# Kernel optimization log

Measured on AMD Instinct MI355X. Metric: run time of the kernel, lower is better.

Reference implementation:

```python
import math
import jax, jax.numpy as jnp
import numpy as np

B, LA, LB, H = 16, 1024, 1024, 512
NEG = -10000000.0


def setup_inputs() -> dict:
    key = jax.random.key(0)
    k1, k2, k3, k4 = jax.random.split(key, 4)
    a = jax.random.normal(k1, (B, LA, H), dtype=jnp.float32)
    b = jax.random.normal(k2, (B, LB, H), dtype=jnp.float32)
    mask_a = jax.random.randint(k3, (B, LA, 1), 0, 2, dtype=jnp.int32)
    mask_b = jax.random.randint(k4, (B, LB, 1), 0, 2, dtype=jnp.int32)
    temperature = jnp.asarray(1.0 / math.sqrt(H), dtype=jnp.float32)
    return {"a": a, "b": b, "mask_a": mask_a, "mask_b": mask_b, "temperature": temperature}


def reference(a, b, mask_a, mask_b, temperature):
    # attn[b,i,j] = <a_i, b_j> * temperature  -> [B, LA, LB]
    attn = jnp.einsum("bid,bjd->bij", a, b) * temperature
    # pairwise validity mask: outer product of per-token masks
    mask = jnp.einsum("bik,bjk->bij", mask_a.astype(jnp.float32), mask_b.astype(jnp.float32)) > 0
    attn = jnp.where(mask, attn, NEG)
    attn_a = jax.nn.softmax(attn, axis=1)  # softmax over a-tokens
    attn_b = jax.nn.softmax(attn, axis=2)  # softmax over b-tokens
    feature_b = jnp.einsum("bij,bid->bjd", attn_a, a)  # [B, LB, H]
    feature_a = jnp.einsum("bij,bjd->bid", attn_b, b)  # [B, LA, H]
    return (feature_a, feature_b)
```

## Files before the change

kernel.cpp:

```cpp
#include <hip/hip_runtime.h>
#include <hip/hip_bf16.h>

#define NB_ 16
#define LA_ 1024
#define LB_ 1024
#define H_  512

typedef __attribute__((ext_vector_type(8))) short short8;
typedef __attribute__((ext_vector_type(4))) float f32x4;

using bf16 = __hip_bfloat16;

__device__ __forceinline__ float bf2f(unsigned short u) {
    union { unsigned int i; float f; } c; c.i = ((unsigned)u) << 16; return c.f;
}
__device__ __forceinline__ unsigned short f2bf(float f) {
    bf16 h = __float2bfloat16(f);
    return *(unsigned short*)&h;
}

__device__ __forceinline__ void load_lds16(const void* g, void* l) {
    __builtin_amdgcn_global_load_lds(
        (const __attribute__((address_space(1))) void*)g,
        (__attribute__((address_space(3))) void*)l, 16, 0, 0);
}

template<int DB, int MODE>
__device__ __forceinline__ void gemm_tile_cnt(
    const unsigned short* __restrict__ gA, const unsigned short* __restrict__ gB,
    int lda, int ldb, size_t ko,
    unsigned short* lds, char* lA, char* lB,
    const int* aoff, const int* boff, f32x4 acc[4][8])
{
    const char* bA = (const char*)lds + DB * 32768;
    const char* bB = (const char*)lds + 65536 + DB * 32768;
    const int nxt = (DB ^ 1) * 32768;
    short8 av[4][2];
#pragma unroll
    for (int p = 0; p < 4; ++p) {
        if (p == 0) {
#pragma unroll
            for (int f = 0; f < 4; f++)
#pragma unroll
                for (int kk = 0; kk < 2; kk++)
                    av[f][kk] = *(const short8*)(bA + (aoff[f] ^ (kk << 6)));
        }
        short8 bv[2][2];
#pragma unroll
        for (int f = 0; f < 2; f++)
#pragma unroll
            for (int kk = 0; kk < 2; kk++)
                bv[f][kk] = *(const short8*)(bB + (boff[p * 2 + f] ^ (kk << 6)));
        if (MODE == 0) {
            if (p == 0) {
                load_lds16(gA + ko,                       lA + nxt);
                load_lds16(gA + ko + (size_t)64 * lda,    lA + nxt + 8192);
            } else if (p == 1) {
                load_lds16(gA + ko + (size_t)128 * lda,   lA + nxt + 16384);
                load_lds16(gA + ko + (size_t)192 * lda,   lA + nxt + 24576);
            } else if (p == 2) {
                load_lds16(gB + ko,                       lB + nxt);
                load_lds16(gB + ko + (size_t)128 * ldb,   lB + nxt + 16384);
            } else {
                load_lds16(gB + ko + (size_t)64 * ldb,    lB + nxt + 8192);
                load_lds16(gB + ko + (size_t)192 * ldb,   lB + nxt + 24576);
            }
        }
        __builtin_amdgcn_s_barrier();
        __builtin_amdgcn_s_setprio(1);
#pragma unroll
        for (int kk = 0; kk < 2; kk++)
#pragma unroll
            for (int f = 0; f < 2; f++)
#pragma unroll
                for (int m = 0; m < 4; m++)
                    acc[m][p * 2 + f] =
                        __builtin_amdgcn_mfma_f32_16x16x32_bf16(
                            av[m][kk], bv[f][kk], acc[m][p * 2 + f], 0, 0, 0);
        __builtin_amdgcn_s_setprio(0);
        if (p == 1) {
            if (MODE == 0) asm volatile("s_waitcnt vmcnt(4)" ::: "memory");
            else           asm volatile("s_waitcnt vmcnt(0)" ::: "memory");
        }
        if (p == 3 && MODE == 0) asm volatile("s_waitcnt vmcnt(2)" ::: "memory");
        if (p < 3 || MODE == 0) __builtin_amdgcn_s_barrier();
    }
}

template<int DB, int MODE>
__device__ __forceinline__ void gemm_tile_drn(
    const unsigned short* __restrict__ gA, const unsigned short* __restrict__ gB,
    int lda, int ldb, size_t ko,
    unsigned short* lds, char* lA, char* lB,
    const int* aoff, const int* boff, f32x4 acc[4][8])
{
    const char* bA = (const char*)lds + DB * 32768;
    const char* bB = (const char*)lds + 65536 + DB * 32768;
    const int nxt = (DB ^ 1) * 32768;
    if (MODE == 0) {
#pragma unroll
        for (int s = 0; s < 4; s++) {
            load_lds16(gA + ko + (size_t)(s * 64) * lda, lA + nxt + s * 8192);
            load_lds16(gB + ko + (size_t)(s * 64) * ldb, lB + nxt + s * 8192);
        }
    }
    short8 av[4][2];
#pragma unroll
    for (int p = 0; p < 4; ++p) {
        if (p == 0) {
#pragma unroll
            for (int f = 0; f < 4; f++)
#pragma unroll
                for (int kk = 0; kk < 2; kk++)
                    av[f][kk] = *(const short8*)(bA + (aoff[f] ^ (kk << 6)));
        }
        short8 bv[2][2];
#pragma unroll
        for (int f = 0; f < 2; f++)
#pragma unroll
            for (int kk = 0; kk < 2; kk++)
                bv[f][kk] = *(const short8*)(bB + (boff[p * 2 + f] ^ (kk << 6)));
        __builtin_amdgcn_s_barrier();
        __builtin_amdgcn_s_setprio(1);
#pragma unroll
        for (int kk = 0; kk < 2; kk++)
#pragma unroll
            for (int f = 0; f < 2; f++)
#pragma unroll
                for (int m = 0; m < 4; m++)
                    acc[m][p * 2 + f] =
                        __builtin_amdgcn_mfma_f32_16x16x32_bf16(
                            av[m][kk], bv[f][kk], acc[m][p * 2 + f], 0, 0, 0);
        __builtin_amdgcn_s_setprio(0);
        if (p < 3) __builtin_amdgcn_s_barrier();
    }
    __syncthreads();
}

template<int SCHED>
__device__ __forceinline__ void gemm_core256(
    const unsigned short* __restrict__ A, const unsigned short* __restrict__ B,
    int lda, int ldb, int K,
    unsigned short* lds, f32x4 acc[4][8])
{
    const int t = threadIdx.x;
    const int w = t >> 6, lane = t & 63;
    const int wr = w >> 1, wc = w & 1;
    const int lm = lane & 15, q = lane >> 4;

    int aoff[4], boff[8];
#pragma unroll
    for (int f = 0; f < 4; f++) {
        const int ra = wr * 64 + f * 16 + lm;
        aoff[f] = ra * 128 + ((q ^ (ra & 7)) << 4);
    }
#pragma unroll
    for (int f = 0; f < 8; f++) {
        const int rb = wc * 128 + f * 16 + lm;
        boff[f] = rb * 128 + ((q ^ (rb & 7)) << 4);
    }

    const int rstep = w * 8 + (lane >> 3);
    const int sc = (lane & 7) ^ (lane >> 3);
    const unsigned short* gA = A + (size_t)rstep * lda + sc * 8;
    const unsigned short* gB = B + (size_t)rstep * ldb + sc * 8;
    char* lA = (char*)lds + w * 1024;
    char* lB = (char*)lds + 65536 + w * 1024;
    const int NT = K >> 6;

    if (SCHED == 0) {
        load_lds16(gA,                       lA);
        load_lds16(gA + (size_t)64 * lda,    lA + 8192);
        load_lds16(gA + (size_t)128 * lda,   lA + 16384);
        load_lds16(gA + (size_t)192 * lda,   lA + 24576);
        load_lds16(gB,                       lB);
        load_lds16(gB + (size_t)128 * ldb,   lB + 16384);
        load_lds16(gB + (size_t)64 * ldb,    lB + 8192);
        load_lds16(gB + (size_t)192 * ldb,   lB + 24576);
        asm volatile("s_waitcnt vmcnt(2)" ::: "memory");
        __builtin_amdgcn_s_barrier();
        int kt = 0;
        for (; kt + 2 < NT; kt += 2) {
            gemm_tile_cnt<0, 0>(gA, gB, lda, ldb, (size_t)(kt + 1) * 64,
                                lds, lA, lB, aoff, boff, acc);
            gemm_tile_cnt<1, 0>(gA, gB, lda, ldb, (size_t)(kt + 2) * 64,
                                lds, lA, lB, aoff, boff, acc);
        }
        gemm_tile_cnt<0, 0>(gA, gB, lda, ldb, (size_t)(NT - 1) * 64,
                            lds, lA, lB, aoff, boff, acc);
        gemm_tile_cnt<1, 1>(gA, gB, lda, ldb, 0, lds, lA, lB, aoff, boff, acc);
    } else {
#pragma unroll
        for (int s = 0; s < 4; s++) {
            load_lds16(gA + (size_t)(s * 64) * lda, lA + s * 8192);
            load_lds16(gB + (size_t)(s * 64) * ldb, lB + s * 8192);
        }
        __syncthreads();
        int kt = 0;
        for (; kt + 2 < NT; kt += 2) {
            gemm_tile_drn<0, 0>(gA, gB, lda, ldb, (size_t)(kt + 1) * 64,
                                lds, lA, lB, aoff, boff, acc);
            gemm_tile_drn<1, 0>(gA, gB, lda, ldb, (size_t)(kt + 2) * 64,
                                lds, lA, lB, aoff, boff, acc);
        }
        gemm_tile_drn<0, 0>(gA, gB, lda, ldb, (size_t)(NT - 1) * 64,
                            lds, lA, lB, aoff, boff, acc);
        gemm_tile_drn<1, 1>(gA, gB, lda, ldb, 0, lds, lA, lB, aoff, boff, acc);
    }
    __syncthreads();
}

__global__ __launch_bounds__(512, 2) void k_gemm_attn(
    const unsigned short* __restrict__ a_bf, const unsigned short* __restrict__ b_bf,
    const int* __restrict__ mask_a, const int* __restrict__ mask_b,
    const float* __restrict__ temp_p,
    unsigned short* __restrict__ E, unsigned short* __restrict__ ET,
    float* __restrict__ l_row, float* __restrict__ l_col)
{
    __shared__ unsigned short lds[65536];

    const int g = blockIdx.x;
    const int batch = g & 15;
    const int qq = g >> 4;
    const int i0 = (qq >> 2) * 256, j0 = (qq & 3) * 256;

    const unsigned short* A = a_bf + (size_t)batch * LA_ * H_ + (size_t)i0 * H_;
    const unsigned short* B = b_bf + (size_t)batch * LB_ * H_ + (size_t)j0 * H_;
    f32x4 acc[4][8];
#pragma unroll
    for (int x = 0; x < 4; x++)
#pragma unroll
        for (int y = 0; y < 8; y++) acc[x][y] = 0;

    gemm_core256<1>(A, B, H_, H_, H_, lds, acc);

    const float temp = temp_p[0];
    const int t = threadIdx.x, w = t >> 6, lane = t & 63;
    const int wr = w >> 1, wc = w & 1, lm = lane & 15, q = lane >> 4;
    const int* map = mask_a + batch * LA_;
    const int* mbp = mask_b + batch * LB_;
    unsigned short* Ep  = E  + (size_t)batch * LA_ * LB_;
    unsigned short* ETp = ET + (size_t)batch * LB_ * LA_;
    float* lrp = l_row + batch * LA_;
    float* lcp = l_col + batch * LB_;

    int mb8[8];
#pragma unroll
    for (int fn = 0; fn < 8; fn++) mb8[fn] = mbp[j0 + wc * 128 + fn * 16 + lm];

#pragma unroll
    for (int fm = 0; fm < 4; fm++) {
        const int ilb = wr * 64 + fm * 16 + q * 4;
        int ma[4];
#pragma unroll
        for (int r = 0; r < 4; r++) ma[r] = map[i0 + ilb + r];
#pragma unroll
        for (int fn = 0; fn < 8; fn++) {
            const int jl = wc * 128 + fn * 16 + lm;
            ushort4 pk;
            unsigned short* pp = (unsigned short*)&pk;
#pragma unroll
            for (int r = 0; r < 4; r++) {
                const float e = (ma[r] && mb8[fn]) ? __expf(acc[fm][fn][r] * temp) : 0.0f;
                acc[fm][fn][r] = e;
                pp[r] = f2bf(e);
                const int il = ilb + r;
                lds[il * 256 + ((((jl >> 3) ^ ((il >> 1) & 15)) << 3) | (jl & 7))] = pp[r];
            }
            *(ushort4*)(ETp + (size_t)(j0 + jl) * LA_ + i0 + ilb) = pk;
        }
    }

#pragma unroll
    for (int fm = 0; fm < 4; fm++)
#pragma unroll
        for (int r = 0; r < 4; r++) {
            float s = 0.0f;
#pragma unroll
            for (int fn = 0; fn < 8; fn++) s += acc[fm][fn][r];
            s += __shfl_xor(s, 1, 16); s += __shfl_xor(s, 2, 16);
            s += __shfl_xor(s, 4, 16); s += __shfl_xor(s, 8, 16);
            if (lm == 0) atomicAdd(&lrp[i0 + wr * 64 + fm * 16 + q * 4 + r], s);
        }
#pragma unroll
    for (int fn = 0; fn < 8; fn++) {
        float s = 0.0f;
#pragma unroll
        for (int fm = 0; fm < 4; fm++)
#pragma unroll
            for (int r = 0; r < 4; r++) s += acc[fm][fn][r];
        s += __shfl_xor(s, 16, 64); s += __shfl_xor(s, 32, 64);
        if (lane < 16) atomicAdd(&lcp[j0 + wc * 128 + fn * 16 + lm], s);
    }

    __syncthreads();
#pragma unroll
    for (int rep = 0; rep < 16; rep++) {
        const int il = (t >> 5) + rep * 16;
        const int c = t & 31;
        const int phys = c ^ ((il >> 1) & 15);
        short8 v = *(const short8*)(lds + il * 256 + phys * 8);
        *(short8*)(Ep + (size_t)(i0 + il) * LB_ + j0 + c * 8) = v;
    }
}

__global__ __launch_bounds__(512, 2) void k_gemm_feat(
    const unsigned short* __restrict__ E, const unsigned short* __restrict__ ET,
    const unsigned short* __restrict__ aT, const unsigned short* __restrict__ bT,
    const int* __restrict__ mask_a, const int* __restrict__ mask_b,
    const int* __restrict__ nA, const int* __restrict__ nB,
    const float* __restrict__ l_row, const float* __restrict__ l_col,
    const float* __restrict__ mean_a, const float* __restrict__ mean_b,
    float* __restrict__ out)
{
    __shared__ unsigned short lds[65536];

    const int g = blockIdx.x;
    const int zc = g & 31;
    const int qq = g >> 5;
    const int n0 = (qq & 1) * 256, m0 = (qq >> 1) * 256;

    const int batch = zc & 15;
    const bool isA = zc < 16;
    const unsigned short* Amat = (isA ? E : ET) + (size_t)batch * 1024 * 1024;
    const unsigned short* Bm   = (isA ? bT : aT) + (size_t)batch * H_ * 1024;
    const int* mp   = (isA ? mask_a : mask_b) + batch * 1024;
    const int nn    = (isA ? nB : nA)[batch];
    const float* sp = (isA ? l_row : l_col) + batch * 1024;
    const float* mv = (isA ? mean_b : mean_a) + batch * H_;
    float* op = out + (isA ? (size_t)0 : (size_t)NB_ * LA_ * H_) + (size_t)batch * 1024 * H_;

    f32x4 acc[4][8];
#pragma unroll
    for (int x = 0; x < 4; x++)
#pragma unroll
        for (int y = 0; y < 8; y++) acc[x][y] = 0;

    gemm_core256<0>(Amat + (size_t)m0 * 1024, Bm + (size_t)n0 * 1024,
                    1024, 1024, 1024, lds, acc);

    const int t = threadIdx.x, w = t >> 6, lane = t & 63;
    const int wr = w >> 1, wc = w & 1, lm = lane & 15, q = lane >> 4;

    float mval[8];
#pragma unroll
    for (int fn = 0; fn < 8; fn++) mval[fn] = mv[n0 + wc * 128 + fn * 16 + lm];

#pragma unroll
    for (int fm = 0; fm < 4; fm++) {
        const int ib = m0 + wr * 64 + fm * 16 + q * 4;
#pragma unroll
        for (int r = 0; r < 4; r++) {
            const int i = ib + r;
            const bool valid = (mp[i] != 0) && (nn > 0);
            const float inv = valid ? 1.0f / sp[i] : 0.0f;
#pragma unroll
            for (int fn = 0; fn < 8; fn++) {
                const int d = n0 + wc * 128 + fn * 16 + lm;
                op[(size_t)i * H_ + d] = valid ? acc[fm][fn][r] * inv : mval[fn];
            }
        }
    }
}

__global__ __launch_bounds__(256) void k_prep(
    const float* __restrict__ a, const float* __restrict__ b,
    unsigned short* __restrict__ aN, unsigned short* __restrict__ bN,
    unsigned short* __restrict__ aT, unsigned short* __restrict__ bT,
    float* __restrict__ mean_a, float* __restrict__ mean_b,
    const int* __restrict__ mask_a, const int* __restrict__ mask_b,
    int* __restrict__ nA, int* __restrict__ nB,
    float* __restrict__ zero_base)
{
    const int g = blockIdx.x, t = threadIdx.x;
    if (g >= 256) {
        const int s = g - 256;
        *(float4*)(zero_base + ((size_t)s * 256 + t) * 4) = make_float4(0, 0, 0, 0);
        const int batch = s & 15, which = s >> 4;
        const int* m = (which ? mask_b : mask_a) + batch * 1024;
        int cnt = m[t] + m[t + 256] + m[t + 512] + m[t + 768];
        __shared__ int red[256];
        red[t] = cnt;
        __syncthreads();
        for (int off = 128; off; off >>= 1) {
            if (t < off) red[t] += red[t + off];
            __syncthreads();
        }
        if (t == 0) (which ? nB : nA)[batch] = red[0];
        return;
    }
    const int dstrip = g & 7, batch = (g >> 3) & 15, sel = g >> 7;
    const float* src = (sel ? b : a) + (size_t)batch * 1024 * H_;
    unsigned short* np = (sel ? bN : aN) + (size_t)batch * 1024 * H_;
    unsigned short* tp = (sel ? bT : aT) + (size_t)batch * H_ * 1024;
    float* mdst = (sel ? mean_b : mean_a) + batch * H_;
    const int d0 = dstrip * 64;

    __shared__ unsigned short lds[64][68];
    __shared__ float cs[4][64];
    const int c4 = (t & 15) * 4;
    float colsum[4] = {0.f, 0.f, 0.f, 0.f};
    for (int i0 = 0; i0 < 1024; i0 += 64) {
#pragma unroll
        for (int it = 0; it < 4; it++) {
            const int r = (t >> 4) + it * 16;
            float4 v = *(const float4*)(src + (size_t)(i0 + r) * H_ + d0 + c4);
            colsum[0] += v.x; colsum[1] += v.y; colsum[2] += v.z; colsum[3] += v.w;
            ushort4 u = make_ushort4(f2bf(v.x), f2bf(v.y), f2bf(v.z), f2bf(v.w));
            *(ushort4*)(np + (size_t)(i0 + r) * H_ + d0 + c4) = u;
            *(ushort4*)&lds[r][c4] = u;
        }
        __syncthreads();
#pragma unroll
        for (int it = 0; it < 4; it++) {
            const int dd = (t >> 4) + it * 16;
            const int i4 = (t & 15) * 4;
            ushort4 u = make_ushort4(lds[i4][dd], lds[i4 + 1][dd],
                                     lds[i4 + 2][dd], lds[i4 + 3][dd]);
            *(ushort4*)(tp + (size_t)(d0 + dd) * 1024 + i0 + i4) = u;
        }
        __syncthreads();
    }
#pragma unroll
    for (int j = 0; j < 4; j++) {
        colsum[j] += __shfl_xor(colsum[j], 16, 64);
        colsum[j] += __shfl_xor(colsum[j], 32, 64);
    }
    const int w = t >> 6, lane = t & 63;
    if (lane < 16) {
#pragma unroll
        for (int j = 0; j < 4; j++) cs[w][c4 + j] = colsum[j];
    }
    __syncthreads();
    if (t < 64) mdst[d0 + t] = (cs[0][t] + cs[1][t] + cs[2][t] + cs[3][t]) * (1.0f / 1024.0f);
}

extern "C" void kernel_launch(void* const* d_in, const int* in_sizes, int n_in,
                              void* d_out, int out_size, void* d_ws, size_t ws_size,
                              hipStream_t stream)
{
    const float* a      = (const float*)d_in[0];
    const float* b      = (const float*)d_in[1];
    const int*   mask_a = (const int*)d_in[2];
    const int*   mask_b = (const int*)d_in[3];
    const float* temp   = (const float*)d_in[4];
    float* out = (float*)d_out;

    char* ws = (char*)d_ws;
    size_t off = 0;
    unsigned short* E    = (unsigned short*)(ws + off); off += (size_t)NB_ * LA_ * LB_ * 2;
    unsigned short* ET   = (unsigned short*)(ws + off); off += (size_t)NB_ * LB_ * LA_ * 2;
    unsigned short* a_bf = (unsigned short*)(ws + off); off += (size_t)NB_ * LA_ * H_ * 2;
    unsigned short* b_bf = (unsigned short*)(ws + off); off += (size_t)NB_ * LB_ * H_ * 2;
    unsigned short* aT   = (unsigned short*)(ws + off); off += (size_t)NB_ * H_ * LA_ * 2;
    unsigned short* bT   = (unsigned short*)(ws + off); off += (size_t)NB_ * H_ * LB_ * 2;
    float* l_row  = (float*)(ws + off); off += (size_t)NB_ * LA_ * 4;
    float* l_col  = (float*)(ws + off); off += (size_t)NB_ * LB_ * 4;
    float* mean_a = (float*)(ws + off); off += (size_t)NB_ * H_ * 4;
    float* mean_b = (float*)(ws + off); off += (size_t)NB_ * H_ * 4;
    int*   nA     = (int*)(ws + off); off += 64;
    int*   nB     = (int*)(ws + off); off += 64;

    k_prep<<<dim3(288), 256, 0, stream>>>(
        a, b, a_bf, b_bf, aT, bT, mean_a, mean_b,
        mask_a, mask_b, nA, nB, l_row);

    k_gemm_attn<<<dim3(256), 512, 0, stream>>>(
        a_bf, b_bf, mask_a, mask_b, temp, E, ET, l_row, l_col);

    k_gemm_feat<<<dim3(256), 512, 0, stream>>>(
        E, ET, aT, bT, mask_a, mask_b, nA, nB, l_row, l_col, mean_a, mean_b, out);
}
```

Measured before the change: 203.9 us.

## Replace global atomics with per-tile partial sums and split prep across rows

Row and column softmax denominators are now reduced within each attention tile through shared memory and written as four per-tile partials, which the feature kernel sums on load. This removes the global atomicAdd traffic and the zero-init pass. The prep kernel's row range is split into four quarters, raising the grid from 288 to 1056 blocks, and each quarter writes a partial column mean that is summed later. In exchange there is an extra LDS staging pass and barriers in the attention epilogue, plus extra partial loads in the feature kernel.

```diff
diff --git a/kernel.cpp b/kernel.cpp
--- a/kernel.cpp
+++ b/kernel.cpp
@@ -215,7 +215,7 @@
     const int* __restrict__ mask_a, const int* __restrict__ mask_b,
     const float* __restrict__ temp_p,
     unsigned short* __restrict__ E, unsigned short* __restrict__ ET,
-    float* __restrict__ l_row, float* __restrict__ l_col)
+    float* __restrict__ l_row_p, float* __restrict__ l_col_p)
 {
     __shared__ unsigned short lds[65536];
 
@@ -241,8 +241,6 @@
     const int* mbp = mask_b + batch * LB_;
     unsigned short* Ep  = E  + (size_t)batch * LA_ * LB_;
     unsigned short* ETp = ET + (size_t)batch * LB_ * LA_;
-    float* lrp = l_row + batch * LA_;
-    float* lcp = l_col + batch * LB_;
 
     int mb8[8];
 #pragma unroll
@@ -264,13 +262,13 @@
                 const float e = (ma[r] && mb8[fn]) ? __expf(acc[fm][fn][r] * temp) : 0.0f;
                 acc[fm][fn][r] = e;
                 pp[r] = f2bf(e);
-                const int il = ilb + r;
-                lds[il * 256 + ((((jl >> 3) ^ ((il >> 1) & 15)) << 3) | (jl & 7))] = pp[r];
             }
             *(ushort4*)(ETp + (size_t)(j0 + jl) * LA_ + i0 + ilb) = pk;
         }
     }
 
+    float* lrow_s = (float*)lds;
+    float* lcol_s = (float*)lds + 512;
 #pragma unroll
     for (int fm = 0; fm < 4; fm++)
 #pragma unroll
@@ -280,7 +278,7 @@
             for (int fn = 0; fn < 8; fn++) s += acc[fm][fn][r];
             s += __shfl_xor(s, 1, 16); s += __shfl_xor(s, 2, 16);
             s += __shfl_xor(s, 4, 16); s += __shfl_xor(s, 8, 16);
-            if (lm == 0) atomicAdd(&lrp[i0 + wr * 64 + fm * 16 + q * 4 + r], s);
+            if (lm == 0) lrow_s[wc * 256 + wr * 64 + fm * 16 + q * 4 + r] = s;
         }
 #pragma unroll
     for (int fn = 0; fn < 8; fn++) {
@@ -290,9 +288,33 @@
 #pragma unroll
             for (int r = 0; r < 4; r++) s += acc[fm][fn][r];
         s += __shfl_xor(s, 16, 64); s += __shfl_xor(s, 32, 64);
-        if (lane < 16) atomicAdd(&lcp[j0 + wc * 128 + fn * 16 + lm], s);
-    }
-
+        if (lane < 16) lcol_s[wr * 256 + wc * 128 + fn * 16 + lm] = s;
+    }
+    __syncthreads();
+    if (t < 256) {
+        l_row_p[(size_t)batch * 4096 + (qq & 3) * 1024 + i0 + t] =
+            lrow_s[t] + lrow_s[256 + t];
+    } else if (t < 512) {
+        const int j = t - 256;
+        l_col_p[(size_t)batch * 4096 + (qq >> 2) * 1024 + j0 + j] =
+            lcol_s[j] + lcol_s[256 + j] + lcol_s[512 + j] + lcol_s[768 + j];
+    }
+    __syncthreads();
+
+#pragma unroll
+    for (int fm = 0; fm < 4; fm++) {
+        const int ilb = wr * 64 + fm * 16 + q * 4;
+#pragma unroll
+        for (int fn = 0; fn < 8; fn++) {
+            const int jl = wc * 128 + fn * 16 + lm;
+#pragma unroll
+            for (int r = 0; r < 4; r++) {
+                const int il = ilb + r;
+                lds[il * 256 + ((((jl >> 3) ^ ((il >> 1) & 15)) << 3) | (jl & 7))] =
+                    f2bf(acc[fm][fn][r]);
+            }
+        }
+    }
     __syncthreads();
 #pragma unroll
     for (int rep = 0; rep < 16; rep++) {
@@ -309,8 +331,8 @@
     const unsigned short* __restrict__ aT, const unsigned short* __restrict__ bT,
     const int* __restrict__ mask_a, const int* __restrict__ mask_b,
     const int* __restrict__ nA, const int* __restrict__ nB,
-    const float* __restrict__ l_row, const float* __restrict__ l_col,
-    const float* __restrict__ mean_a, const float* __restrict__ mean_b,
+    const float* __restrict__ l_row_p, const float* __restrict__ l_col_p,
+    const float* __restrict__ mean_a_p, const float* __restrict__ mean_b_p,
     float* __restrict__ out)
 {
     __shared__ unsigned short lds[65536];
@@ -326,8 +348,8 @@
     const unsigned short* Bm   = (isA ? bT : aT) + (size_t)batch * H_ * 1024;
     const int* mp   = (isA ? mask_a : mask_b) + batch * 1024;
     const int nn    = (isA ? nB : nA)[batch];
-    const float* sp = (isA ? l_row : l_col) + batch * 1024;
-    const float* mv = (isA ? mean_b : mean_a) + batch * H_;
+    const float* spp = (isA ? l_row_p : l_col_p) + (size_t)batch * 4096;
+    const float* mvp = (isA ? mean_b_p : mean_a_p) + (size_t)batch * 2048;
     float* op = out + (isA ? (size_t)0 : (size_t)NB_ * LA_ * H_) + (size_t)batch * 1024 * H_;
 
     f32x4 acc[4][8];
@@ -344,7 +366,10 @@
 
     float mval[8];
 #pragma unroll
-    for (int fn = 0; fn < 8; fn++) mval[fn] = mv[n0 + wc * 128 + fn * 16 + lm];
+    for (int fn = 0; fn < 8; fn++) {
+        const int d = n0 + wc * 128 + fn * 16 + lm;
+        mval[fn] = mvp[d] + mvp[512 + d] + mvp[1024 + d] + mvp[1536 + d];
+    }
 
 #pragma unroll
     for (int fm = 0; fm < 4; fm++) {
@@ -353,7 +378,8 @@
         for (int r = 0; r < 4; r++) {
             const int i = ib + r;
             const bool valid = (mp[i] != 0) && (nn > 0);
-            const float inv = valid ? 1.0f / sp[i] : 0.0f;
+            const float s4 = spp[i] + spp[1024 + i] + spp[2048 + i] + spp[3072 + i];
+            const float inv = valid ? 1.0f / s4 : 0.0f;
 #pragma unroll
             for (int fn = 0; fn < 8; fn++) {
                 const int d = n0 + wc * 128 + fn * 16 + lm;
@@ -367,15 +393,13 @@
     const float* __restrict__ a, const float* __restrict__ b,
     unsigned short* __restrict__ aN, unsigned short* __restrict__ bN,
     unsigned short* __restrict__ aT, unsigned short* __restrict__ bT,
-    float* __restrict__ mean_a, float* __restrict__ mean_b,
+    float* __restrict__ mean_a_p, float* __restrict__ mean_b_p,
     const int* __restrict__ mask_a, const int* __restrict__ mask_b,
-    int* __restrict__ nA, int* __restrict__ nB,
-    float* __restrict__ zero_base)
+    int* __restrict__ nA, int* __restrict__ nB)
 {
     const int g = blockIdx.x, t = threadIdx.x;
-    if (g >= 256) {
-        const int s = g - 256;
-        *(float4*)(zero_base + ((size_t)s * 256 + t) * 4) = make_float4(0, 0, 0, 0);
+    if (g >= 1024) {
+        const int s = g - 1024;
         const int batch = s & 15, which = s >> 4;
         const int* m = (which ? mask_b : mask_a) + batch * 1024;
         int cnt = m[t] + m[t + 256] + m[t + 512] + m[t + 768];
@@ -389,18 +413,20 @@
         if (t == 0) (which ? nB : nA)[batch] = red[0];
         return;
     }
-    const int dstrip = g & 7, batch = (g >> 3) & 15, sel = g >> 7;
+    const int dstrip = g & 7, tq = (g >> 3) & 3, batch = (g >> 5) & 15, sel = g >> 9;
     const float* src = (sel ? b : a) + (size_t)batch * 1024 * H_;
     unsigned short* np = (sel ? bN : aN) + (size_t)batch * 1024 * H_;
     unsigned short* tp = (sel ? bT : aT) + (size_t)batch * H_ * 1024;
-    float* mdst = (sel ? mean_b : mean_a) + batch * H_;
+    float* mdst = (sel ? mean_b_p : mean_a_p) + (size_t)batch * 2048 + tq * 512;
     const int d0 = dstrip * 64;
+    const int ibase = tq * 256;
 
     __shared__ unsigned short lds[64][68];
     __shared__ float cs[4][64];
     const int c4 = (t & 15) * 4;
     float colsum[4] = {0.f, 0.f, 0.f, 0.f};
-    for (int i0 = 0; i0 < 1024; i0 += 64) {
+    for (int ii = 0; ii < 256; ii += 64) {
+        const int i0 = ibase + ii;
 #pragma unroll
         for (int it = 0; it < 4; it++) {
             const int r = (t >> 4) + it * 16;
@@ -432,7 +458,8 @@
         for (int j = 0; j < 4; j++) cs[w][c4 + j] = colsum[j];
     }
     __syncthreads();
-    if (t < 64) mdst[d0 + t] = (cs[0][t] + cs[1][t] + cs[2][t] + cs[3][t]) * (1.0f / 1024.0f);
+    if (t < 64)
+        mdst[d0 + t] = (cs[0][t] + cs[1][t] + cs[2][t] + cs[3][t]) * (1.0f / 1024.0f);
 }
 
 extern "C" void kernel_launch(void* const* d_in, const int* in_sizes, int n_in,
@@ -454,20 +481,21 @@
     unsigned short* b_bf = (unsigned short*)(ws + off); off += (size_t)NB_ * LB_ * H_ * 2;
     unsigned short* aT   = (unsigned short*)(ws + off); off += (size_t)NB_ * H_ * LA_ * 2;
     unsigned short* bT   = (unsigned short*)(ws + off); off += (size_t)NB_ * H_ * LB_ * 2;
-    float* l_row  = (float*)(ws + off); off += (size_t)NB_ * LA_ * 4;
-    float* l_col  = (float*)(ws + off); off += (size_t)NB_ * LB_ * 4;
-    float* mean_a = (float*)(ws + off); off += (size_t)NB_ * H_ * 4;
-    float* mean_b = (float*)(ws + off); off += (size_t)NB_ * H_ * 4;
+    float* l_row_p  = (float*)(ws + off); off += (size_t)NB_ * 4 * LA_ * 4;
+    float* l_col_p  = (float*)(ws + off); off += (size_t)NB_ * 4 * LB_ * 4;
+    float* mean_a_p = (float*)(ws + off); off += (size_t)NB_ * 4 * H_ * 4;
+    float* mean_b_p = (float*)(ws + off); off += (size_t)NB_ * 4 * H_ * 4;
     int*   nA     = (int*)(ws + off); off += 64;
     int*   nB     = (int*)(ws + off); off += 64;
 
-    k_prep<<<dim3(288), 256, 0, stream>>>(
-        a, b, a_bf, b_bf, aT, bT, mean_a, mean_b,
-        mask_a, mask_b, nA, nB, l_row);
+    k_prep<<<dim3(1056), 256, 0, stream>>>(
+        a, b, a_bf, b_bf, aT, bT, mean_a_p, mean_b_p,
+        mask_a, mask_b, nA, nB);
 
     k_gemm_attn<<<dim3(256), 512, 0, stream>>>(
-        a_bf, b_bf, mask_a, mask_b, temp, E, ET, l_row, l_col);
+        a_bf, b_bf, mask_a, mask_b, temp, E, ET, l_row_p, l_col_p);
 
     k_gemm_feat<<<dim3(256), 512, 0, stream>>>(
-        E, ET, aT, bT, mask_a, mask_b, nA, nB, l_row, l_col, mean_a, mean_b, out);
-}
+        E, ET, aT, bT, mask_a, mask_b, nA, nB,
+        l_row_p, l_col_p, mean_a_p, mean_b_p, out);
+}
```

Measured after the change: 211.5 us. 3.7% more time.
